# Optimization experiments

Hardware: AMD Instinct MI355X
Metric: run time of the kernel (lower is better)

Reference implementation:

```python
import jax, jax.numpy as jnp
import numpy as np

B, N, F_IN, F_OUT = 64, 1024, 200, 200
NEG_SLOPE = 0.2  # PyG GATConv default


def setup_inputs() -> dict:
    key = jax.random.key(0)
    k1, k2, k3, k4, k5 = jax.random.split(key, 5)
    return {
        "x": jax.random.normal(k1, (B, 1, N, F_IN), dtype=jnp.float32),
        "W": jax.random.normal(k2, (F_IN, F_OUT), dtype=jnp.float32) * 0.05,
        "att_src": jax.random.normal(k3, (F_OUT,), dtype=jnp.float32) * 0.05,
        "att_dst": jax.random.normal(k4, (F_OUT,), dtype=jnp.float32) * 0.05,
        "bias": jax.random.normal(k5, (F_OUT,), dtype=jnp.float32) * 0.05,
    }


def reference(x, W, att_src, att_dst, bias):
    # x: [B, 1, N, F_IN]; module flattens to (B*N) nodes but the edge_index
    # only spans node ids 0..N-1 (complete graph minus self loops). PyG's
    # GATConv re-adds self loops for ALL B*N nodes, so:
    #   nodes 0..N-1 : dense softmax attention over all N nodes (incl. self)
    #   nodes >= N   : only the self loop -> out = h_i + bias
    b, _, n, f = x.shape
    xf = x.reshape(b * n, f)
    h = xf @ W                                # [B*N, F_OUT] linear transform

    h0 = h[:n]                                # first graph's nodes
    a_s = h0 @ att_src                        # [N] per-source score
    a_d = h0 @ att_dst                        # [N] per-target score
    # score[i, j] = leaky_relu(a_dst[i] + a_src[j]), softmax over sources j
    scores = jax.nn.leaky_relu(a_d[:, None] + a_s[None, :], negative_slope=NEG_SLOPE)
    alpha = jax.nn.softmax(scores, axis=1)    # [N, N]
    out0 = alpha @ h0 + bias                  # [N, F_OUT]

    out_rest = h[n:] + bias                   # self-loop only -> alpha == 1
    out = jnp.concatenate([out0, out_rest], axis=0)
    return out.reshape(b, n, -1)[:, None]     # [B, 1, N, F_OUT]
```

## Files before the change

kernel.cpp:

```cpp
#include <hip/hip_runtime.h>

#define BATCH 64
#define NNODE 1024
#define FDIM  200
#define MROWS (BATCH * NNODE)
#define NEG_SLOPE 0.2f

#define NKT 7
#define NNT 13
#define KTBYTES (NNT * 1024)

typedef short s16x8 __attribute__((ext_vector_type(8)));
typedef float f32x4 __attribute__((ext_vector_type(4)));


__device__ __forceinline__ unsigned int f2bf(float f) {
    unsigned int u = __float_as_uint(f);
    return (u + 0x7fffu + ((u >> 16) & 1u)) >> 16;
}
__device__ __forceinline__ unsigned int pack2(float a, float b) {
    return f2bf(a) | (f2bf(b) << 16);
}
__device__ __forceinline__ float lrelu(float s) {
    return (s > 0.f) ? s : NEG_SLOPE * s;
}

__global__ __launch_bounds__(64) void k_prep(const float* __restrict__ W,
                                             const float* __restrict__ att_src,
                                             const float* __restrict__ att_dst,
                                             unsigned short* __restrict__ fragW,
                                             float* __restrict__ wsv,
                                             float* __restrict__ wdv)
{
    const int b    = blockIdx.x;
    const int lane = threadIdx.x;

    if (b < 91) {
        const int kt   = b / NNT;
        const int nt   = b - kt * NNT;
        const int n    = nt * 16 + (lane & 15);
        const int kb   = kt * 32 + (lane >> 4) * 8;
        s16x8 v;
        #pragma unroll
        for (int j = 0; j < 8; ++j) {
            int k = kb + j;
            float f = (k < FDIM && n < FDIM) ? W[k * FDIM + n] : 0.f;
            v[j] = (short)f2bf(f);
        }
        ((s16x8*)(fragW + (size_t)b * 512))[lane] = v;
    } else {
        const int kk = b - 91;
        const float* Wr = W + kk * FDIM;
        float ps = 0.f, pd = 0.f;
        #pragma unroll
        for (int i = 0; i < 4; ++i) {
            int n = lane + i * 64;
            if (n < FDIM) {
                float wv = Wr[n];
                ps = fmaf(wv, att_src[n], ps);
                pd = fmaf(wv, att_dst[n], pd);
            }
        }
        #pragma unroll
        for (int off = 32; off; off >>= 1) {
            ps += __shfl_down(ps, off);
            pd += __shfl_down(pd, off);
        }
        if (lane == 0) { wsv[kk] = ps; wdv[kk] = pd; }
    }
}

__global__ __launch_bounds__(256, 4) void k_gemm(const float* __restrict__ x,
                                                 const unsigned short* __restrict__ fragW,
                                                 const float* __restrict__ bias,
                                                 const float* __restrict__ wsv,
                                                 const float* __restrict__ wdv,
                                                 float* __restrict__ out,
                                                 unsigned short* __restrict__ h0frag,
                                                 float* __restrict__ a_s,
                                                 float* __restrict__ a_d)
{
    __shared__ __align__(16) unsigned short Bs[2][KTBYTES / 2];
    const int tid  = threadIdx.x;
    const int lane = tid & 63;
    const int w    = __builtin_amdgcn_readfirstlane(tid >> 6);
    const int ln   = lane & 15;
    const int quad = lane >> 4;
    const int R0   = blockIdx.x * 64;
    const int row0 = R0 + w * 16;

#define STAGE(kt_, buf_)                                                      \
    {                                                                         \
        const char* gsrc = (const char*)fragW + (size_t)(kt_) * KTBYTES;      \
        char* lbase = (char*)&Bs[buf_][0];                                    \
        _Pragma("unroll")                                                     \
        for (int i = 0; i < 4; ++i) {                                         \
            int g = i * 4 + w;                                                \
            if (g < NNT)                                                      \
                __builtin_amdgcn_global_load_lds(                             \
                    (const __attribute__((address_space(1))) void*)           \
                        (gsrc + g * 1024 + lane * 16),                        \
                    (__attribute__((address_space(3))) void*)                 \
                        (lbase + g * 1024),                                   \
                    16, 0, 0);                                                \
        }                                                                     \
    }

#define LOADA(p_, slot_)                                                      \
    {                                                                         \
        if ((p_) < 6) {                                                       \
            const float4* ap = (const float4*)(xrow + (p_) * 32 + quad * 8);  \
            ar[slot_][0] = ap[0]; ar[slot_][1] = ap[1];                       \
        } else {                                                              \
            if (quad == 0) {                                                  \
                const float4* ap = (const float4*)(xrow + (p_) * 32);         \
                ar[slot_][0] = ap[0]; ar[slot_][1] = ap[1];                   \
            } else {                                                          \
                ar[slot_][0] = make_float4(0.f, 0.f, 0.f, 0.f);               \
                ar[slot_][1] = make_float4(0.f, 0.f, 0.f, 0.f);               \
            }                                                                 \
        }                                                                     \
    }

    f32x4 acc[NNT];
    #pragma unroll
    for (int nt = 0; nt < NNT; ++nt) acc[nt] = (f32x4){0.f, 0.f, 0.f, 0.f};

    const float* xrow = x + (size_t)(row0 + ln) * FDIM;
    float4 ar[2][2];

    LOADA(0, 0);
    STAGE(0, 0);
    __syncthreads();

    #pragma unroll
    for (int kt = 0; kt < NKT; ++kt) {
        const int cur = kt & 1;
        if (kt < NKT - 1) {
            STAGE(kt + 1, cur ^ 1);
            LOADA(kt + 1, cur ^ 1);
        }
        float4 f0 = ar[cur][0], f1 = ar[cur][1];
        unsigned int au[4] = {pack2(f0.x, f0.y), pack2(f0.z, f0.w),
                              pack2(f1.x, f1.y), pack2(f1.z, f1.w)};
        s16x8 a = *(s16x8*)au;
        const unsigned short* bbase = &Bs[cur][0];
        #pragma unroll
        for (int nt = 0; nt < NNT; ++nt) {
            s16x8 b = *(const s16x8*)(bbase + nt * 512 + lane * 8);
            acc[nt] = __builtin_amdgcn_mfma_f32_16x16x32_bf16(a, b, acc[nt], 0, 0, 0);
        }
        if (kt < NKT - 1) __syncthreads();
    }
#undef STAGE
#undef LOADA

    if (R0 >= NNODE) {
        #pragma unroll
        for (int nt = 0; nt < NNT; ++nt) {
            int col = nt * 16 + ln;
            if (nt < 12 || ln < 8) {
                float bv = bias[col];
                #pragma unroll
                for (int r = 0; r < 4; ++r)
                    out[(size_t)(row0 + quad * 4 + r) * FDIM + col] = acc[nt][r] + bv;
            }
        }
    } else {
        {
            float ps = 0.f, pd = 0.f;
            #pragma unroll
            for (int kt = 0; kt < NKT; ++kt) {
                if (kt < 6 || quad == 0) {
                    const float4* ap = (const float4*)(xrow + kt * 32 + quad * 8);
                    float4 f0 = ap[0], f1 = ap[1];
                    const float4* sp = (const float4*)(wsv + kt * 32 + quad * 8);
                    const float4* dp = (const float4*)(wdv + kt * 32 + quad * 8);
                    float4 s0 = sp[0], s1 = sp[1], d0 = dp[0], d1 = dp[1];
                    ps += f0.x*s0.x + f0.y*s0.y + f0.z*s0.z + f0.w*s0.w
                        + f1.x*s1.x + f1.y*s1.y + f1.z*s1.z + f1.w*s1.w;
                    pd += f0.x*d0.x + f0.y*d0.y + f0.z*d0.z + f0.w*d0.w
                        + f1.x*d1.x + f1.y*d1.y + f1.z*d1.z + f1.w*d1.w;
                }
            }
            ps += __shfl_down(ps, 32); ps += __shfl_down(ps, 16);
            pd += __shfl_down(pd, 32); pd += __shfl_down(pd, 16);
            if (lane < 16) {
                a_s[row0 + lane] = ps;
                a_d[row0 + lane] = pd;
            }
        }
        __syncthreads();
        float* scrw = (float*)&Bs[0][0] + w * (16 * 17);
        const int kt2 = row0 >> 5;
        const int lo  = (row0 >> 4) & 1;
        for (int nt = 0; nt < NNT; ++nt) {
            #pragma unroll
            for (int r = 0; r < 4; ++r) scrw[(quad * 4 + r) * 17 + ln] = acc[nt][r];
            __syncthreads();
            if (lane < 32) {
                int oct = lane >> 4, nl = lane & 15;
                uint4 dv;
                dv.x = pack2(scrw[(oct * 8 + 0) * 17 + nl], scrw[(oct * 8 + 1) * 17 + nl]);
                dv.y = pack2(scrw[(oct * 8 + 2) * 17 + nl], scrw[(oct * 8 + 3) * 17 + nl]);
                dv.z = pack2(scrw[(oct * 8 + 4) * 17 + nl], scrw[(oct * 8 + 5) * 17 + nl]);
                dv.w = pack2(scrw[(oct * 8 + 6) * 17 + nl], scrw[(oct * 8 + 7) * 17 + nl]);
                *(uint4*)(h0frag + ((size_t)(kt2 * NNT + nt) * 64 + lo * 32 + lane) * 8) = dv;
            }
            __syncthreads();
        }
    }
}

__global__ __launch_bounds__(256) void k_attn(const unsigned short* __restrict__ h0frag,
                                              const float* __restrict__ a_s,
                                              const float* __restrict__ a_d,
                                              const float* __restrict__ bias,
                                              float* __restrict__ out)
{
    __shared__ __align__(16) float as_s[1024];
    __shared__ float mls[16];
    __shared__ float rls[16];
    __shared__ f32x4 red[3][64];
    const int tid  = threadIdx.x;
    const int lane = tid & 63;
    const int w    = __builtin_amdgcn_readfirstlane(tid >> 6);
    const int ln   = lane & 15;
    const int quad = lane >> 4;
    const int it   = blockIdx.x / NNT;
    const int nt   = blockIdx.x - it * NNT;
    const int i0   = it * 16;

    #pragma unroll
    for (int i = 0; i < 4; ++i) as_s[tid + i * 256] = a_s[tid + i * 256];
    __syncthreads();

    float mx = -1e30f;
    #pragma unroll
    for (int i = 0; i < 16; ++i) mx = fmaxf(mx, as_s[lane + i * 64]);
    #pragma unroll
    for (int off = 32; off; off >>= 1) mx = fmaxf(mx, __shfl_down(mx, off));
    mx = __shfl(mx, 0);

    #pragma unroll
    for (int rr = 0; rr < 4; ++rr) {
        const int r  = w * 4 + rr;
        const float adr = a_d[i0 + r];
        const float mi  = lrelu(adr + mx);
        float sum = 0.f;
        #pragma unroll
        for (int i = 0; i < 16; ++i)
            sum += __expf(lrelu(adr + as_s[lane + i * 64]) - mi);
        #pragma unroll
        for (int off = 32; off; off >>= 1) sum += __shfl_down(sum, off);
        if (lane == 0) { mls[r] = mi; rls[r] = 1.0f / sum; }
    }
    __syncthreads();

    const float ad = a_d[i0 + ln];
    const float mi = mls[ln];

    f32x4 accA = (f32x4){0.f, 0.f, 0.f, 0.f};
    f32x4 accB = (f32x4){0.f, 0.f, 0.f, 0.f};

    #pragma unroll
    for (int k8 = 0; k8 < 8; ++k8) {
        const int kt2 = w * 8 + k8;
        const float4* ap = (const float4*)(as_s + kt2 * 32 + quad * 8);
        float4 f0 = ap[0], f1 = ap[1];
        float e[8] = {f0.x, f0.y, f0.z, f0.w, f1.x, f1.y, f1.z, f1.w};
        #pragma unroll
        for (int j = 0; j < 8; ++j)
            e[j] = __expf(lrelu(ad + e[j]) - mi);
        unsigned int au[4] = {pack2(e[0], e[1]), pack2(e[2], e[3]),
                              pack2(e[4], e[5]), pack2(e[6], e[7])};
        s16x8 afrag = *(s16x8*)au;
        s16x8 b = *(const s16x8*)(h0frag + ((size_t)(kt2 * NNT + nt) * 64 + lane) * 8);
        if (k8 & 1) accB = __builtin_amdgcn_mfma_f32_16x16x32_bf16(afrag, b, accB, 0, 0, 0);
        else        accA = __builtin_amdgcn_mfma_f32_16x16x32_bf16(afrag, b, accA, 0, 0, 0);
    }

    f32x4 acc = accA + accB;
    if (w > 0) red[w - 1][lane] = acc;
    __syncthreads();

    if (w == 0) {
        #pragma unroll
        for (int ww = 0; ww < 3; ++ww) acc += red[ww][lane];
        const int col = nt * 16 + ln;
        if (nt < 12 || ln < 8) {
            float bv = bias[col];
            #pragma unroll
            for (int r = 0; r < 4; ++r) {
                float rl = rls[quad * 4 + r];
                out[(size_t)(i0 + quad * 4 + r) * FDIM + col] = acc[r] * rl + bv;
            }
        }
    }
}

extern "C" void kernel_launch(void* const* d_in, const int* in_sizes, int n_in,
                              void* d_out, int out_size, void* d_ws, size_t ws_size,
                              hipStream_t stream)
{
    const float* x       = (const float*)d_in[0];
    const float* W       = (const float*)d_in[1];
    const float* att_src = (const float*)d_in[2];
    const float* att_dst = (const float*)d_in[3];
    const float* bias    = (const float*)d_in[4];
    float* out = (float*)d_out;
    char*  wsb = (char*)d_ws;

    unsigned short* h0frag = (unsigned short*)(wsb + 0);
    float* a_s   = (float*)(wsb + 425984);
    float* a_d   = (float*)(wsb + 430080);
    unsigned short* fragW = (unsigned short*)(wsb + 442368);
    float* wsv   = (float*)(wsb + 535552);
    float* wdv   = (float*)(wsb + 536352);

    k_prep <<<291,         64, 0, stream>>>(W, att_src, att_dst, fragW, wsv, wdv);
    k_gemm <<<MROWS / 64, 256, 0, stream>>>(x, fragW, bias, wsv, wdv, out, h0frag, a_s, a_d);
    k_attn <<<64 * NNT,   256, 0, stream>>>(h0frag, a_s, a_d, bias, out);
}
```

Before: 132.3 us.

## Stage full bf16 W into LDS once per block and preload all x fragments

k_gemm now uses 512-thread blocks over 128 rows. It copies the whole 91KB fragment-packed W into shared memory in one pass instead of double-buffering one K-slab at a time with a barrier per step. All seven x fragments are loaded into registers up front and reused for the attention-score dot products instead of being reloaded from global memory. This removes the per-k-step barriers and the duplicate x reads. In exchange it uses about 100KB of LDS per block, which limits occupancy, and holds more registers, with no overlap between the W load and compute.

```diff
diff --git a/kernel.cpp b/kernel.cpp
--- a/kernel.cpp
+++ b/kernel.cpp
@@ -8,7 +8,7 @@
 
 #define NKT 7
 #define NNT 13
-#define KTBYTES (NNT * 1024)
+#define FRAGW_BYTES (NKT * NNT * 1024)
 
 typedef short s16x8 __attribute__((ext_vector_type(8)));
 typedef float f32x4 __attribute__((ext_vector_type(4)));
@@ -70,7 +70,7 @@
     }
 }
 
-__global__ __launch_bounds__(256, 4) void k_gemm(const float* __restrict__ x,
+__global__ __launch_bounds__(512, 2) void k_gemm(const float* __restrict__ x,
                                                  const unsigned short* __restrict__ fragW,
                                                  const float* __restrict__ bias,
                                                  const float* __restrict__ wsv,
@@ -80,80 +80,67 @@
                                                  float* __restrict__ a_s,
                                                  float* __restrict__ a_d)
 {
-    __shared__ __align__(16) unsigned short Bs[2][KTBYTES / 2];
+    __shared__ __align__(16) unsigned short Bf[FRAGW_BYTES / 2];
+    __shared__ float scr[8][16 * 17];
     const int tid  = threadIdx.x;
     const int lane = tid & 63;
     const int w    = __builtin_amdgcn_readfirstlane(tid >> 6);
     const int ln   = lane & 15;
     const int quad = lane >> 4;
-    const int R0   = blockIdx.x * 64;
+    const int R0   = blockIdx.x * 128;
     const int row0 = R0 + w * 16;
 
-#define STAGE(kt_, buf_)                                                      \
-    {                                                                         \
-        const char* gsrc = (const char*)fragW + (size_t)(kt_) * KTBYTES;      \
-        char* lbase = (char*)&Bs[buf_][0];                                    \
-        _Pragma("unroll")                                                     \
-        for (int i = 0; i < 4; ++i) {                                         \
-            int g = i * 4 + w;                                                \
-            if (g < NNT)                                                      \
-                __builtin_amdgcn_global_load_lds(                             \
-                    (const __attribute__((address_space(1))) void*)           \
-                        (gsrc + g * 1024 + lane * 16),                        \
-                    (__attribute__((address_space(3))) void*)                 \
-                        (lbase + g * 1024),                                   \
-                    16, 0, 0);                                                \
-        }                                                                     \
-    }
-
-#define LOADA(p_, slot_)                                                      \
-    {                                                                         \
-        if ((p_) < 6) {                                                       \
-            const float4* ap = (const float4*)(xrow + (p_) * 32 + quad * 8);  \
-            ar[slot_][0] = ap[0]; ar[slot_][1] = ap[1];                       \
-        } else {                                                              \
-            if (quad == 0) {                                                  \
-                const float4* ap = (const float4*)(xrow + (p_) * 32);         \
-                ar[slot_][0] = ap[0]; ar[slot_][1] = ap[1];                   \
-            } else {                                                          \
-                ar[slot_][0] = make_float4(0.f, 0.f, 0.f, 0.f);               \
-                ar[slot_][1] = make_float4(0.f, 0.f, 0.f, 0.f);               \
-            }                                                                 \
-        }                                                                     \
+    {
+        const char* gsrc = (const char*)fragW;
+        char* ldst = (char*)&Bf[0];
+        #pragma unroll
+        for (int r = 0; r < 12; ++r) {
+            int off = tid * 16 + r * 8192;
+            if (off < FRAGW_BYTES)
+                __builtin_amdgcn_global_load_lds(
+                    (const __attribute__((address_space(1))) void*)(gsrc + off),
+                    (__attribute__((address_space(3))) void*)(ldst + off),
+                    16, 0, 0);
+        }
+    }
+
+    const float* xrow = x + (size_t)(row0 + ln) * FDIM;
+    float4 ar[NKT][2];
+    #pragma unroll
+    for (int kt = 0; kt < NKT; ++kt) {
+        if (kt < 6) {
+            const float4* ap = (const float4*)(xrow + kt * 32 + quad * 8);
+            ar[kt][0] = ap[0]; ar[kt][1] = ap[1];
+        } else {
+            if (quad == 0) {
+                const float4* ap = (const float4*)(xrow + kt * 32);
+                ar[kt][0] = ap[0]; ar[kt][1] = ap[1];
+            } else {
+                ar[kt][0] = make_float4(0.f, 0.f, 0.f, 0.f);
+                ar[kt][1] = make_float4(0.f, 0.f, 0.f, 0.f);
+            }
+        }
     }
 
     f32x4 acc[NNT];
     #pragma unroll
     for (int nt = 0; nt < NNT; ++nt) acc[nt] = (f32x4){0.f, 0.f, 0.f, 0.f};
 
-    const float* xrow = x + (size_t)(row0 + ln) * FDIM;
-    float4 ar[2][2];
-
-    LOADA(0, 0);
-    STAGE(0, 0);
     __syncthreads();
 
     #pragma unroll
     for (int kt = 0; kt < NKT; ++kt) {
-        const int cur = kt & 1;
-        if (kt < NKT - 1) {
-            STAGE(kt + 1, cur ^ 1);
-            LOADA(kt + 1, cur ^ 1);
-        }
-        float4 f0 = ar[cur][0], f1 = ar[cur][1];
+        float4 f0 = ar[kt][0], f1 = ar[kt][1];
         unsigned int au[4] = {pack2(f0.x, f0.y), pack2(f0.z, f0.w),
                               pack2(f1.x, f1.y), pack2(f1.z, f1.w)};
         s16x8 a = *(s16x8*)au;
-        const unsigned short* bbase = &Bs[cur][0];
+        const unsigned short* bbase = &Bf[kt * NNT * 512];
         #pragma unroll
         for (int nt = 0; nt < NNT; ++nt) {
             s16x8 b = *(const s16x8*)(bbase + nt * 512 + lane * 8);
             acc[nt] = __builtin_amdgcn_mfma_f32_16x16x32_bf16(a, b, acc[nt], 0, 0, 0);
         }
-        if (kt < NKT - 1) __syncthreads();
-    }
-#undef STAGE
-#undef LOADA
+    }
 
     if (R0 >= NNODE) {
         #pragma unroll
@@ -172,8 +159,7 @@
             #pragma unroll
             for (int kt = 0; kt < NKT; ++kt) {
                 if (kt < 6 || quad == 0) {
-                    const float4* ap = (const float4*)(xrow + kt * 32 + quad * 8);
-                    float4 f0 = ap[0], f1 = ap[1];
+                    float4 f0 = ar[kt][0], f1 = ar[kt][1];
                     const float4* sp = (const float4*)(wsv + kt * 32 + quad * 8);
                     const float4* dp = (const float4*)(wdv + kt * 32 + quad * 8);
                     float4 s0 = sp[0], s1 = sp[1], d0 = dp[0], d1 = dp[1];
@@ -190,8 +176,7 @@
                 a_d[row0 + lane] = pd;
             }
         }
-        __syncthreads();
-        float* scrw = (float*)&Bs[0][0] + w * (16 * 17);
+        float* scrw = &scr[w][0];
         const int kt2 = row0 >> 5;
         const int lo  = (row0 >> 4) & 1;
         for (int nt = 0; nt < NNT; ++nt) {
@@ -318,7 +303,7 @@
     float* wsv   = (float*)(wsb + 535552);
     float* wdv   = (float*)(wsb + 536352);
 
-    k_prep <<<291,         64, 0, stream>>>(W, att_src, att_dst, fragW, wsv, wdv);
-    k_gemm <<<MROWS / 64, 256, 0, stream>>>(x, fragW, bias, wsv, wdv, out, h0frag, a_s, a_d);
-    k_attn <<<64 * NNT,   256, 0, stream>>>(h0frag, a_s, a_d, bias, out);
-}
+    k_prep <<<291,          64, 0, stream>>>(W, att_src, att_dst, fragW, wsv, wdv);
+    k_gemm <<<MROWS / 128, 512, 0, stream>>>(x, fragW, bias, wsv, wdv, out, h0frag, a_s, a_d);
+    k_attn <<<64 * NNT,    256, 0, stream>>>(h0frag, a_s, a_d, bias, out);
+}
```

Measured after the change: 128.5 us. -2.8%, faster.
